# Performance work log

Measured on AMD Instinct MI355X. Metric: run time of the kernel, lower is better.

The kernel has to match this reference:

```python
import jax, jax.numpy as jnp
import numpy as np
from jax import lax
from jax.scipy.stats import norm

KERNLEN = 31
NSIG = 4
EPS = 1e-3


def _gkern(kernlen=KERNLEN, nsig=NSIG):
    # Faithful port of HA._gkern (scipy.stats.norm.cdf -> jax.scipy.stats.norm.cdf)
    interval = (2.0 * nsig + 1.0) / kernlen
    x = jnp.linspace(-nsig - interval / 2.0, nsig + interval / 2.0, kernlen + 1)
    kern1d = jnp.diff(norm.cdf(x))
    kernel_raw = jnp.sqrt(jnp.outer(kern1d, kern1d))
    kernel = kernel_raw / kernel_raw.sum()
    return kernel.astype(jnp.float32)


def setup_inputs() -> dict:
    key = jax.random.key(0)
    attention = jax.random.uniform(key, (64, 1, 512, 512), dtype=jnp.float32)
    gaussian_kernel = _gkern()[None, None, :, :]  # OIHW [1,1,31,31]
    return {"attention": attention, "gaussian_kernel": gaussian_kernel}


def reference(attention, gaussian_kernel):
    a = jnp.clip(attention, 0.0, 1.0)
    # single-channel 31x31 conv, 'same' padding (pad 15)
    soft = lax.conv_general_dilated(
        a, gaussian_kernel,
        window_strides=(1, 1),
        padding=[(15, 15), (15, 15)],
        dimension_numbers=("NCHW", "OIHW", "NCHW"),
    )
    # per-image min-max normalization over H,W (per (n,c) slice)
    mx = soft.max(axis=(2, 3), keepdims=True)
    mn = soft.min(axis=(2, 3), keepdims=True)
    soft = (soft - mn) / jnp.maximum(mx - mn, EPS)  # torch.clamp(max-min, min=eps)
    soft = jnp.nan_to_num(soft, nan=0.0, posinf=1.0, neginf=0.0)
    return jnp.maximum(soft, a)
```

## Files before the change

### kernel.cpp

```cpp
#include <hip/hip_runtime.h>
#include <math.h>

#define IMGS 64
#define HWDIM 512
#define KLEN 31
#define RAD 15
#define EPSV 1e-3f
#define MM_STRIDE 32


__global__ __launch_bounds__(128) void init_k(const float* __restrict__ gk,
                                              float* __restrict__ w,
                                              int* __restrict__ mm) {
    int t = threadIdx.x;
    if (t < KLEN) w[t] = sqrtf(gk[t * KLEN + t]);
    if (t < IMGS) { mm[t * MM_STRIDE] = 0x7F800000; mm[t * MM_STRIDE + 1] = 0; }
}

template <bool EDGE>
__device__ __forceinline__ void loadA(int i, const float* __restrict__ src,
                                      int x0, int y0, float4* __restrict__ b) {
    const int r = i >> 2, q = i & 3;
    int y = y0 - RAD + r;
    if (EDGE) y = y < 0 ? 0 : (y > HWDIM - 1 ? HWDIM - 1 : y);
    const float4* row = (const float4*)(src + ((size_t)y << 9));
    const int gb = (x0 >> 2) + (q << 2) - 4;
#pragma unroll
    for (int m = 0; m < 12; ++m) {
        int g = gb + m;
        if (EDGE) g = g < 0 ? 0 : (g > 127 ? 127 : g);
        b[m] = row[g];
    }
}

template <bool EDGE>
__device__ __forceinline__ void compA(int i, int x0, int y0,
                                      const float* __restrict__ wg,
                                      float* __restrict__ inter,
                                      const float4* __restrict__ b) {
    const int r = i >> 2, q = i & 3;
    const int y = y0 - RAD + r;
    const int gb = (x0 >> 2) + (q << 2) - 4;
    const bool vy = !EDGE || ((unsigned)y < HWDIM);
    float vv[48];
#pragma unroll
    for (int m = 0; m < 12; ++m) {
        const bool vx = !EDGE || (vy && ((unsigned)(gb + m) < 128u));
        vv[4 * m + 0] = vx ? fminf(fmaxf(b[m].x, 0.f), 1.f) : 0.f;
        vv[4 * m + 1] = vx ? fminf(fmaxf(b[m].y, 0.f), 1.f) : 0.f;
        vv[4 * m + 2] = vx ? fminf(fmaxf(b[m].z, 0.f), 1.f) : 0.f;
        vv[4 * m + 3] = vx ? fminf(fmaxf(b[m].w, 0.f), 1.f) : 0.f;
    }
    float* dst = &inter[r * 64 + (q << 4)];
#pragma unroll
    for (int d = 0; d < 4; ++d) {
        float4 o;
        float* op = &o.x;
#pragma unroll
        for (int s = 0; s < 4; ++s) {
            const int oc = (d << 2) + s;
            float a = 0.f;
#pragma unroll
            for (int k = 0; k < KLEN; ++k) a += vv[oc + 1 + k] * wg[k];
            op[s] = a;
        }
        *(float4*)(dst + (d << 2)) = o;
    }
}

template <bool EDGE>
__device__ __forceinline__ void conv_body(const float* __restrict__ attn,
                                          float* __restrict__ out,
                                          const float* __restrict__ wg,
                                          int* __restrict__ mm,
                                          int img, int x0, int y0,
                                          float* __restrict__ inter,
                                          float* __restrict__ sred) {
    const int t = threadIdx.x;
    const float* src = attn + ((size_t)img << 18);

    {
        float4 bA[12], bB[12];
        const bool hasB = t < 120;
        loadA<EDGE>(t, src, x0, y0, bA);
        if (hasB) loadA<EDGE>(256 + t, src, x0, y0, bB);
        compA<EDGE>(t, x0, y0, wg, inter, bA);
        if (hasB) compA<EDGE>(256 + t, x0, y0, wg, inter, bB);
    }
    __syncthreads();

    const int tx = t & 15;
    const int ty = t >> 4;
    float4 acc[4];
#pragma unroll
    for (int i = 0; i < 4; ++i) acc[i] = make_float4(0.f, 0.f, 0.f, 0.f);
#pragma unroll
    for (int k = 0; k < 34; ++k) {
        const float4 v = *(const float4*)&inter[((ty << 2) + k) * 64 + (tx << 2)];
#pragma unroll
        for (int i = 0; i < 4; ++i) {
            const int j = k - i;
            if (j >= 0 && j < KLEN) {
                const float w = wg[j];
                acc[i].x += v.x * w;
                acc[i].y += v.y * w;
                acc[i].z += v.z * w;
                acc[i].w += v.w * w;
            }
        }
    }
    float* dst = out + ((size_t)img << 18);
    float lmin = INFINITY, lmax = -INFINITY;
#pragma unroll
    for (int i = 0; i < 4; ++i) {
        *(float4*)&dst[(size_t)(y0 + (ty << 2) + i) * HWDIM + x0 + (tx << 2)] = acc[i];
        lmin = fminf(lmin, fminf(fminf(acc[i].x, acc[i].y), fminf(acc[i].z, acc[i].w)));
        lmax = fmaxf(lmax, fmaxf(fmaxf(acc[i].x, acc[i].y), fmaxf(acc[i].z, acc[i].w)));
    }
#pragma unroll
    for (int off = 1; off < 64; off <<= 1) {
        lmin = fminf(lmin, __shfl_xor(lmin, off, 64));
        lmax = fmaxf(lmax, __shfl_xor(lmax, off, 64));
    }
    const int lane = t & 63, wid = t >> 6;
    if (lane == 0) { sred[wid] = lmin; sred[4 + wid] = lmax; }
    __syncthreads();
    if (t == 0) {
        float bmin = fminf(fminf(sred[0], sred[1]), fminf(sred[2], sred[3]));
        float bmax = fmaxf(fmaxf(sred[4], sred[5]), fmaxf(sred[6], sred[7]));
        atomicMin(&mm[img * MM_STRIDE], __float_as_int(bmin));
        atomicMax(&mm[img * MM_STRIDE + 1], __float_as_int(bmax));
    }
}

__global__ __launch_bounds__(256) void conv_k(const float* __restrict__ attn,
                                              float* __restrict__ out,
                                              const float* __restrict__ wg,
                                              int* __restrict__ mm) {
    __shared__ float inter[94 * 64];
    __shared__ float sred[8];
    const int sw  = ((blockIdx.x & 7) << 9) + (blockIdx.x >> 3);
    const int img = sw >> 6;
    const int by  = (sw >> 3) & 7;
    const int bx  = sw & 7;
    const int x0 = bx << 6;
    const int y0 = by << 6;
    if (bx == 0 || bx == 7 || by == 0 || by == 7)
        conv_body<true>(attn, out, wg, mm, img, x0, y0, inter, sred);
    else
        conv_body<false>(attn, out, wg, mm, img, x0, y0, inter, sred);
}

__global__ __launch_bounds__(256) void final_k(const float* __restrict__ attn,
                                               float* __restrict__ out,
                                               const int* __restrict__ mm) {
    const int img = blockIdx.x >> 6;
    const float mn = __int_as_float(mm[img * MM_STRIDE]);
    const float mx = __int_as_float(mm[img * MM_STRIDE + 1]);
    const float inv = 1.0f / fmaxf(mx - mn, EPSV);
    const size_t base0 = ((size_t)blockIdx.x << 12) + ((size_t)threadIdx.x << 2);
#pragma unroll
    for (int h = 0; h < 4; ++h) {
        const size_t base = base0 + (size_t)h * 1024;
        float4 s = *(const float4*)(out + base);
        float4 a = *(const float4*)(attn + base);
        float4 o;
        o.x = fmaxf((s.x - mn) * inv, fminf(fmaxf(a.x, 0.f), 1.f));
        o.y = fmaxf((s.y - mn) * inv, fminf(fmaxf(a.y, 0.f), 1.f));
        o.z = fmaxf((s.z - mn) * inv, fminf(fmaxf(a.z, 0.f), 1.f));
        o.w = fmaxf((s.w - mn) * inv, fminf(fmaxf(a.w, 0.f), 1.f));
        *(float4*)(out + base) = o;
    }
}

extern "C" void kernel_launch(void* const* d_in, const int* in_sizes, int n_in,
                              void* d_out, int out_size, void* d_ws, size_t ws_size,
                              hipStream_t stream) {
    const float* attn = (const float*)d_in[0];
    const float* gk   = (const float*)d_in[1];
    float* out  = (float*)d_out;
    float* wsf  = (float*)d_ws;
    float* w1d  = wsf;
    int*   mm   = (int*)(wsf + 32);

    init_k<<<1, 128, 0, stream>>>(gk, w1d, mm);
    conv_k<<<4096, 256, 0, stream>>>(attn, out, w1d, mm);
    final_k<<<IMGS * HWDIM * HWDIM / 4096, 256, 0, stream>>>(attn, out, mm);
}
```

Before: 79.85 us.

## Stage input tile in LDS via global_load_lds with XOR swizzle, reuse for intermediate

```diff
diff --git a/kernel.cpp b/kernel.cpp
--- a/kernel.cpp
+++ b/kernel.cpp
@@ -1,5 +1,6 @@
 #include <hip/hip_runtime.h>
 #include <math.h>
+#include <stdint.h>
 
 #define IMGS 64
 #define HWDIM 512
@@ -8,6 +9,13 @@
 #define EPSV 1e-3f
 #define MM_STRIDE 32
 
+
+typedef __attribute__((address_space(3))) uint8_t  lds_u8;
+typedef const __attribute__((address_space(1))) uint8_t g_u8;
+
+__device__ __forceinline__ int swz8(int s, int rx) {
+    return (s & ~7) | ((s & 7) ^ rx);
+}
 
 __global__ __launch_bounds__(128) void init_k(const float* __restrict__ gk,
                                               float* __restrict__ w,
@@ -18,30 +26,18 @@
 }
 
 template <bool EDGE>
-__device__ __forceinline__ void loadA(int i, const float* __restrict__ src,
-                                      int x0, int y0, float4* __restrict__ b) {
-    const int r = i >> 2, q = i & 3;
-    int y = y0 - RAD + r;
-    if (EDGE) y = y < 0 ? 0 : (y > HWDIM - 1 ? HWDIM - 1 : y);
-    const float4* row = (const float4*)(src + ((size_t)y << 9));
-    const int gb = (x0 >> 2) + (q << 2) - 4;
+__device__ __forceinline__ void itemA(int i, int x0, int y0,
+                                      const float* __restrict__ wg,
+                                      float* __restrict__ raw) {
+    const int r = i >> 2, q = i & 3, rx = r & 7;
+    const int sb = q << 2;
+    float4 b[12];
 #pragma unroll
-    for (int m = 0; m < 12; ++m) {
-        int g = gb + m;
-        if (EDGE) g = g < 0 ? 0 : (g > 127 ? 127 : g);
-        b[m] = row[g];
-    }
-}
-
-template <bool EDGE>
-__device__ __forceinline__ void compA(int i, int x0, int y0,
-                                      const float* __restrict__ wg,
-                                      float* __restrict__ inter,
-                                      const float4* __restrict__ b) {
-    const int r = i >> 2, q = i & 3;
+    for (int m = 0; m < 12; ++m)
+        b[m] = *(const float4*)&raw[(r * 24 + swz8(sb + m, rx)) << 2];
     const int y = y0 - RAD + r;
-    const int gb = (x0 >> 2) + (q << 2) - 4;
     const bool vy = !EDGE || ((unsigned)y < HWDIM);
+    const int gb = (x0 >> 2) - 4 + sb;
     float vv[48];
 #pragma unroll
     for (int m = 0; m < 12; ++m) {
@@ -51,7 +47,6 @@
         vv[4 * m + 2] = vx ? fminf(fmaxf(b[m].z, 0.f), 1.f) : 0.f;
         vv[4 * m + 3] = vx ? fminf(fmaxf(b[m].w, 0.f), 1.f) : 0.f;
     }
-    float* dst = &inter[r * 64 + (q << 4)];
 #pragma unroll
     for (int d = 0; d < 4; ++d) {
         float4 o;
@@ -64,7 +59,7 @@
             for (int k = 0; k < KLEN; ++k) a += vv[oc + 1 + k] * wg[k];
             op[s] = a;
         }
-        *(float4*)(dst + (d << 2)) = o;
+        *(float4*)&raw[(r * 24 + swz8(4 + sb + d, rx)) << 2] = o;
     }
 }
 
@@ -74,19 +69,30 @@
                                           const float* __restrict__ wg,
                                           int* __restrict__ mm,
                                           int img, int x0, int y0,
-                                          float* __restrict__ inter,
+                                          float* __restrict__ raw,
                                           float* __restrict__ sred) {
     const int t = threadIdx.x;
     const float* src = attn + ((size_t)img << 18);
 
-    {
-        float4 bA[12], bB[12];
-        const bool hasB = t < 120;
-        loadA<EDGE>(t, src, x0, y0, bA);
-        if (hasB) loadA<EDGE>(256 + t, src, x0, y0, bB);
-        compA<EDGE>(t, x0, y0, wg, inter, bA);
-        if (hasB) compA<EDGE>(256 + t, x0, y0, wg, inter, bB);
+    const int gbq = (x0 >> 2) - 4;
+#pragma unroll
+    for (int it = 0; it < 9; ++it) {
+        const int i  = t + (it << 8);
+        const int ic = i < 2255 ? i : 2255;
+        const int r   = ic / 24;
+        const int c4p = ic - r * 24;
+        const int c4l = (c4p & ~7) | ((c4p & 7) ^ (r & 7));
+        int y = y0 - RAD + r;
+        y = y < 0 ? 0 : (y > HWDIM - 1 ? HWDIM - 1 : y);
+        int g4 = gbq + c4l;
+        g4 = g4 < 0 ? 0 : (g4 > 127 ? 127 : g4);
+        const float* gp = src + ((size_t)y << 9) + (g4 << 2);
+        __builtin_amdgcn_global_load_lds((g_u8*)gp, (lds_u8*)&raw[i << 2], 16, 0, 0);
     }
+    __syncthreads();
+
+    itemA<EDGE>(t, x0, y0, wg, raw);
+    if (t < 120) itemA<EDGE>(256 + t, x0, y0, wg, raw);
     __syncthreads();
 
     const int tx = t & 15;
@@ -96,7 +102,8 @@
     for (int i = 0; i < 4; ++i) acc[i] = make_float4(0.f, 0.f, 0.f, 0.f);
 #pragma unroll
     for (int k = 0; k < 34; ++k) {
-        const float4 v = *(const float4*)&inter[((ty << 2) + k) * 64 + (tx << 2)];
+        const int row = (ty << 2) + k;
+        const float4 v = *(const float4*)&raw[(row * 24 + swz8(4 + tx, row & 7)) << 2];
 #pragma unroll
         for (int i = 0; i < 4; ++i) {
             const int j = k - i;
@@ -137,7 +144,7 @@
                                               float* __restrict__ out,
                                               const float* __restrict__ wg,
                                               int* __restrict__ mm) {
-    __shared__ float inter[94 * 64];
+    __shared__ float raw[2304 * 4];
     __shared__ float sred[8];
     const int sw  = ((blockIdx.x & 7) << 9) + (blockIdx.x >> 3);
     const int img = sw >> 6;
@@ -146,9 +153,9 @@
     const int x0 = bx << 6;
     const int y0 = by << 6;
     if (bx == 0 || bx == 7 || by == 0 || by == 7)
-        conv_body<true>(attn, out, wg, mm, img, x0, y0, inter, sred);
+        conv_body<true>(attn, out, wg, mm, img, x0, y0, raw, sred);
     else
-        conv_body<false>(attn, out, wg, mm, img, x0, y0, inter, sred);
+        conv_body<false>(attn, out, wg, mm, img, x0, y0, raw, sred);
 }
 
 __global__ __launch_bounds__(256) void final_k(const float* __restrict__ attn,
```

New measurement: 82.36 us. 1.03x slower.
